# Optimization experiments

Measured on AMD Instinct MI355X. Metric: run time of the kernel, lower is better.

The kernel has to match this reference:

```python
import jax, jax.numpy as jnp
import numpy as np

EPS = 1e-5
QB = 127.0  # int8 activation quantization bound

def rmsnorm(x):
    # SimpleRMSNorm: x / rms(x), no learned scale
    return x * jax.lax.rsqrt(jnp.mean(x * x, axis=-1, keepdims=True) + EPS)

def activation_quant(x):
    # per-token absmax int8 quant-dequant
    scale = QB / jnp.clip(jnp.max(jnp.abs(x), axis=-1, keepdims=True), EPS)
    return jnp.clip(jnp.round(x * scale), -QB - 1, QB) / scale

def weight_quant(w):
    # per-tensor ternary quant-dequant (BitNet b1.58)
    scale = 1.0 / jnp.clip(jnp.mean(jnp.abs(w)), EPS)
    return jnp.clip(jnp.round(w * scale), -1.0, 1.0) / scale

def ste(x, q):
    # straight-through estimator: forward uses q, gradient flows to x
    return x + jax.lax.stop_gradient(q - x)

def bitlinear(x, w, b):
    xn = rmsnorm(x)
    xq = ste(xn, activation_quant(xn))
    wq = ste(w, weight_quant(w))
    # x: [b, s, d_in], w: [d_out, d_in] -> [b, s, d_out]
    return jnp.einsum('bsd,od->bso', xq, wq) + b

def setup_inputs() -> dict:
    key = jax.random.key(0)
    k1, k2, k3, k4, k5 = jax.random.split(key, 5)
    dim, inner = 1024, 4096
    x = jax.random.normal(k1, (4, 4096, dim), dtype=jnp.float32)
    w1 = jax.random.normal(k2, (inner, dim), dtype=jnp.float32) * (dim ** -0.5)
    b1 = jax.random.normal(k3, (inner,), dtype=jnp.float32) * 0.02
    w2 = jax.random.normal(k4, (dim, inner), dtype=jnp.float32) * (inner ** -0.5)
    b2 = jax.random.normal(k5, (dim,), dtype=jnp.float32) * 0.02
    return {"x": x, "w1": w1, "b1": b1, "w2": w2, "b2": b2}

def reference(x, w1, b1, w2, b2):
    h = jax.nn.gelu(bitlinear(x, w1, b1), approximate=False)  # torch nn.GELU default = exact erf
    # dropout p=0.0 is identity; post_act_ln disabled
    return bitlinear(h, w2, b2)
```

## Files before the change

### kernel.cpp

```cpp
#include <hip/hip_runtime.h>
#include <hip/hip_bf16.h>

#define TOK   16384
#define DIM   1024
#define INNER 4096
#define EPSF  1e-5f

typedef int v4i __attribute__((ext_vector_type(4)));

static __device__ __forceinline__ void async_copy16(const char* g, char* l) {
    __builtin_amdgcn_global_load_lds(
        (const __attribute__((address_space(1))) unsigned int*)g,
        (__attribute__((address_space(3))) unsigned int*)l, 16, 0, 0);
}

static __device__ __forceinline__ float bf2f(unsigned short u) {
    return __uint_as_float(((unsigned)u) << 16);
}
static __device__ __forceinline__ unsigned short f2bf(float f) {
    unsigned u = __float_as_uint(f);
    return (unsigned short)((u + 0x7fffu + ((u >> 16) & 1u)) >> 16);
}

static __device__ __forceinline__ float fast_erf(float z) {
    float az = fabsf(z);
    float tt = __builtin_amdgcn_rcpf(1.f + 0.3275911f * az);
    float poly = ((((1.061405429f * tt - 1.453152027f) * tt + 1.421413741f) * tt
                   - 0.284496736f) * tt + 0.254829592f) * tt;
    float er = 1.f - poly * __expf(-az * az);
    return copysignf(er, z);
}

static __device__ __forceinline__ float waveSum(float v) {
#pragma unroll
    for (int o = 32; o > 0; o >>= 1) v += __shfl_down(v, o, 64);
    return v;
}
static __device__ __forceinline__ float waveMax(float v) {
#pragma unroll
    for (int o = 32; o > 0; o >>= 1) v = fmaxf(v, __shfl_down(v, o, 64));
    return v;
}

__global__ void absmean_k(const float* __restrict__ w, int n4, float* __restrict__ acc) {
    int idx = blockIdx.x * blockDim.x + threadIdx.x;
    int stride = gridDim.x * blockDim.x;
    const float4* w4 = (const float4*)w;
    float s = 0.f;
    for (int i = idx; i < n4; i += stride) {
        float4 v = w4[i];
        s += fabsf(v.x) + fabsf(v.y) + fabsf(v.z) + fabsf(v.w);
    }
    __shared__ float sp[4];
    int wv = threadIdx.x >> 6, lane = threadIdx.x & 63;
    s = waveSum(s);
    if (lane == 0) sp[wv] = s;
    __syncthreads();
    if (threadIdx.x == 0) atomicAdd(acc, sp[0] + sp[1] + sp[2] + sp[3]);
}

__global__ void wquant_k(const float* __restrict__ w, int n,
                         const float* __restrict__ acc, float* __restrict__ wscale,
                         char* __restrict__ wq) {
    float mean = *acc / (float)n;
    float cl = fmaxf(mean, EPSF);
    float s = 1.f / cl;
    if (blockIdx.x == 0 && threadIdx.x == 0) *wscale = cl;
    int idx = blockIdx.x * blockDim.x + threadIdx.x;
    int stride = gridDim.x * blockDim.x;
    int n4 = n >> 2;
    const float4* w4 = (const float4*)w;
    unsigned* q4 = (unsigned*)wq;
    for (int i = idx; i < n4; i += stride) {
        float4 v = w4[i];
        float e[4] = {v.x, v.y, v.z, v.w};
        unsigned packed = 0;
#pragma unroll
        for (int j = 0; j < 4; j++) {
            float r = rintf(e[j] * s);
            r = fminf(fmaxf(r, -1.f), 1.f);
            packed |= ((unsigned)((int)r & 0xff)) << (8 * j);
        }
        q4[i] = packed;
    }
}

template <int D, int VPT>
__global__ void actquant_f32_k(const float* __restrict__ X, char* __restrict__ Q,
                               float* __restrict__ rs_out) {
    int token = blockIdx.x;
    int t = threadIdx.x;
    const float4* xp = (const float4*)(X + (long)token * D);
    float vals[VPT];
    float ss = 0.f, am = 0.f;
#pragma unroll
    for (int j = 0; j < VPT / 4; j++) {
        float4 v = xp[t * (VPT / 4) + j];
        vals[4 * j] = v.x; vals[4 * j + 1] = v.y; vals[4 * j + 2] = v.z; vals[4 * j + 3] = v.w;
        ss += v.x * v.x + v.y * v.y + v.z * v.z + v.w * v.w;
        am = fmaxf(am, fmaxf(fmaxf(fabsf(v.x), fabsf(v.y)), fmaxf(fabsf(v.z), fabsf(v.w))));
    }
    __shared__ float sp[8];
    __shared__ float bc[2];
    int wv = t >> 6, lane = t & 63;
    float S = waveSum(ss);
    float M = waveMax(am);
    if (lane == 0) { sp[wv] = S; sp[4 + wv] = M; }
    __syncthreads();
    if (t == 0) {
        float Sa = sp[0] + sp[1] + sp[2] + sp[3];
        float Ma = fmaxf(fmaxf(sp[4], sp[5]), fmaxf(sp[6], sp[7]));
        float rinv = rsqrtf(Sa * (1.f / (float)D) + EPSF);
        float amn = Ma * rinv;
        float scale = 127.f / fmaxf(amn, EPSF);
        rs_out[token] = 1.f / scale;
        bc[0] = rinv; bc[1] = scale;
    }
    __syncthreads();
    float rinv = bc[0], scale = bc[1];
    unsigned outw[VPT / 4];
#pragma unroll
    for (int j = 0; j < VPT; j++) {
        float r = rintf((vals[j] * rinv) * scale);
        r = fminf(fmaxf(r, -128.f), 127.f);
        unsigned qi = (unsigned)((int)r & 0xff) << (8 * (j & 3));
        if ((j & 3) == 0) outw[j / 4] = qi; else outw[j / 4] |= qi;
    }
    unsigned* qp = (unsigned*)(Q + (long)token * D);
#pragma unroll
    for (int j = 0; j < VPT / 4; j++) qp[t * (VPT / 4) + j] = outw[j];
}

template <int D, int VPT>
__global__ void actquant_bf16_k(const unsigned short* __restrict__ X, char* __restrict__ Q,
                                float* __restrict__ rs_out) {
    int token = blockIdx.x;
    int t = threadIdx.x;
    const unsigned* x2 = (const unsigned*)(X + (long)token * D);
    float vals[VPT];
    float ss = 0.f, am = 0.f;
#pragma unroll
    for (int j = 0; j < VPT / 2; j++) {
        unsigned v = x2[t * (VPT / 2) + j];
        float f0 = bf2f((unsigned short)(v & 0xffff));
        float f1 = bf2f((unsigned short)(v >> 16));
        vals[2 * j] = f0; vals[2 * j + 1] = f1;
        ss += f0 * f0 + f1 * f1;
        am = fmaxf(am, fmaxf(fabsf(f0), fabsf(f1)));
    }
    __shared__ float sp[8];
    __shared__ float bc[2];
    int wv = t >> 6, lane = t & 63;
    float S = waveSum(ss);
    float M = waveMax(am);
    if (lane == 0) { sp[wv] = S; sp[4 + wv] = M; }
    __syncthreads();
    if (t == 0) {
        float Sa = sp[0] + sp[1] + sp[2] + sp[3];
        float Ma = fmaxf(fmaxf(sp[4], sp[5]), fmaxf(sp[6], sp[7]));
        float rinv = rsqrtf(Sa * (1.f / (float)D) + EPSF);
        float amn = Ma * rinv;
        float scale = 127.f / fmaxf(amn, EPSF);
        rs_out[token] = 1.f / scale;
        bc[0] = rinv; bc[1] = scale;
    }
    __syncthreads();
    float rinv = bc[0], scale = bc[1];
    unsigned outw[VPT / 4];
#pragma unroll
    for (int j = 0; j < VPT; j++) {
        float r = rintf((vals[j] * rinv) * scale);
        r = fminf(fmaxf(r, -128.f), 127.f);
        unsigned qi = (unsigned)((int)r & 0xff) << (8 * (j & 3));
        if ((j & 3) == 0) outw[j / 4] = qi; else outw[j / 4] |= qi;
    }
    unsigned* qp = (unsigned*)(Q + (long)token * D);
#pragma unroll
    for (int j = 0; j < VPT / 4; j++) qp[t * (VPT / 4) + j] = outw[j];
}

template <int DO_GELU, int OUT_F32>
__global__ __launch_bounds__(256) void gemm_i8_k(
    const char* __restrict__ A, const char* __restrict__ Bw,
    const float* __restrict__ rs, const float* __restrict__ wscale_p,
    const float* __restrict__ bias, void* __restrict__ outp,
    int M, int N, int K) {
    __shared__ char As[2][8192];
    __shared__ char Bs[2][8192];
    int t = threadIdx.x;
    int n0 = blockIdx.x * 128, m0 = blockIdx.y * 128;
    int wv = t >> 6, lane = t & 63, lm = lane & 15, q = lane >> 4;
    int wrow = (wv >> 1) * 64, wcol = (wv & 1) * 64;

    int r = t >> 2;
    int csrc = (t & 3) ^ (r & 3);
    const char* Ap = A + (long)(m0 + r) * K + csrc * 16;
    const char* Bp = Bw + (long)(n0 + r) * K + csrc * 16;
    long rowoff = (long)64 * K;

    v4i acc[4][4] = {};
    int aidx[4], bidx[4];
#pragma unroll
    for (int i = 0; i < 4; i++) {
        int ml = wrow + i * 16 + lm;
        aidx[i] = ml * 4 + (q ^ (ml & 3));
        int nl = wcol + i * 16 + lm;
        bidx[i] = nl * 4 + (q ^ (nl & 3));
    }

    auto issue = [&](int it, int buf) {
        long k0 = (long)it << 6;
        async_copy16(Ap + k0,          As[buf] + t * 16);
        async_copy16(Ap + rowoff + k0, As[buf] + 4096 + t * 16);
        async_copy16(Bp + k0,          Bs[buf] + t * 16);
        async_copy16(Bp + rowoff + k0, Bs[buf] + 4096 + t * 16);
    };

    int nIt = K >> 6;
    issue(0, 0);
    for (int it = 0; it < nIt; ++it) {
        int cur = it & 1;
        if (it + 1 < nIt) {
            issue(it + 1, cur ^ 1);
            asm volatile("s_waitcnt vmcnt(4)" ::: "memory");
        } else {
            asm volatile("s_waitcnt vmcnt(0)" ::: "memory");
        }
        asm volatile("s_barrier" ::: "memory");
        const v4i* As4 = (const v4i*)As[cur];
        const v4i* Bs4 = (const v4i*)Bs[cur];
        v4i a[4], b[4];
#pragma unroll
        for (int i = 0; i < 4; i++) { a[i] = As4[aidx[i]]; b[i] = Bs4[bidx[i]]; }
#pragma unroll
        for (int i = 0; i < 4; i++)
#pragma unroll
            for (int j = 0; j < 4; j++)
                acc[i][j] = __builtin_amdgcn_mfma_i32_16x16x64_i8(a[i], b[j], acc[i][j], 0, 0, 0);
        asm volatile("s_barrier" ::: "memory");
    }

    float wsc = *wscale_p;
#pragma unroll
    for (int i = 0; i < 4; i++) {
        int mg = m0 + wrow + i * 16 + q * 4;
        float fs[4];
#pragma unroll
        for (int rr = 0; rr < 4; rr++) fs[rr] = rs[mg + rr] * wsc;
#pragma unroll
        for (int j = 0; j < 4; j++) {
            int ng = n0 + wcol + j * 16 + lm;
            float bv = bias[ng];
#pragma unroll
            for (int rr = 0; rr < 4; rr++) {
                float v = (float)acc[i][j][rr] * fs[rr] + bv;
                if (DO_GELU) v = 0.5f * v * (1.f + fast_erf(v * 0.70710678118654752f));
                long idx = (long)(mg + rr) * N + ng;
                if (OUT_F32) ((float*)outp)[idx] = v;
                else ((unsigned short*)outp)[idx] = f2bf(v);
            }
        }
    }
}

extern "C" void kernel_launch(void* const* d_in, const int* in_sizes, int n_in,
                              void* d_out, int out_size, void* d_ws, size_t ws_size,
                              hipStream_t stream) {
    const float* x  = (const float*)d_in[0];
    const float* w1 = (const float*)d_in[1];
    const float* b1 = (const float*)d_in[2];
    const float* w2 = (const float*)d_in[3];
    const float* b2 = (const float*)d_in[4];
    float* out = (float*)d_out;

    char* ws = (char*)d_ws;
    float* acc1 = (float*)(ws + 0);
    float* acc2 = (float*)(ws + 4);
    float* wsc1 = (float*)(ws + 8);
    float* wsc2 = (float*)(ws + 12);
    size_t off = 256;
    char* w1q = ws + off; off += (size_t)INNER * DIM;
    char* w2q = ws + off; off += (size_t)INNER * DIM;
    char* xq1 = ws + off; off += (size_t)TOK * DIM;
    float* rs1 = (float*)(ws + off); off += (size_t)TOK * 4;
    char* xq2 = ws + off; off += (size_t)TOK * INNER;
    float* rs2 = (float*)(ws + off); off += (size_t)TOK * 4;
    unsigned short* h = (unsigned short*)(ws + off);

    hipMemsetAsync(d_ws, 0, 16, stream);

    int nw = INNER * DIM;
    absmean_k<<<1024, 256, 0, stream>>>(w1, nw / 4, acc1);
    absmean_k<<<1024, 256, 0, stream>>>(w2, nw / 4, acc2);
    wquant_k<<<2048, 256, 0, stream>>>(w1, nw, acc1, wsc1, w1q);
    wquant_k<<<2048, 256, 0, stream>>>(w2, nw, acc2, wsc2, w2q);

    actquant_f32_k<DIM, 4><<<TOK, 256, 0, stream>>>(x, xq1, rs1);
    gemm_i8_k<1, 0><<<dim3(INNER / 128, TOK / 128), 256, 0, stream>>>(
        xq1, w1q, rs1, wsc1, b1, (void*)h, TOK, INNER, DIM);
    actquant_bf16_k<INNER, 16><<<TOK, 256, 0, stream>>>(h, xq2, rs2);
    gemm_i8_k<0, 1><<<dim3(DIM / 128, TOK / 128), 256, 0, stream>>>(
        xq2, w2q, rs2, wsc2, b2, (void*)out, TOK, DIM, INNER);
}
```

Measured before the change: 440.0 us.

## Enlarge int8 GEMM tile to 256x128 using 32x32x32 MFMA and vectorize actquant IO

The int8 GEMM tile grows from 128x128 to 256x128, and each wave now computes a 128x64 subtile with 32x32x32 i8 MFMAs instead of 16x16x64. The LDS swizzle and the async copy pattern change to match the larger A tile. This raises arithmetic intensity and reuse of the B tile, at the cost of more accumulator registers and more LDS, and it halves the number of blocks. The bf16 activation-quant kernel also switches to 16-byte vector loads and stores.

```diff
diff --git a/kernel.cpp b/kernel.cpp
--- a/kernel.cpp
+++ b/kernel.cpp
@@ -6,7 +6,8 @@
 #define INNER 4096
 #define EPSF  1e-5f
 
-typedef int v4i __attribute__((ext_vector_type(4)));
+typedef int v4i  __attribute__((ext_vector_type(4)));
+typedef int v16i __attribute__((ext_vector_type(16)));
 
 static __device__ __forceinline__ void async_copy16(const char* g, char* l) {
     __builtin_amdgcn_global_load_lds(
@@ -136,17 +137,21 @@
                                 float* __restrict__ rs_out) {
     int token = blockIdx.x;
     int t = threadIdx.x;
-    const unsigned* x2 = (const unsigned*)(X + (long)token * D);
+    const uint4* xp = (const uint4*)(X + (long)token * D);
     float vals[VPT];
     float ss = 0.f, am = 0.f;
 #pragma unroll
-    for (int j = 0; j < VPT / 2; j++) {
-        unsigned v = x2[t * (VPT / 2) + j];
-        float f0 = bf2f((unsigned short)(v & 0xffff));
-        float f1 = bf2f((unsigned short)(v >> 16));
-        vals[2 * j] = f0; vals[2 * j + 1] = f1;
-        ss += f0 * f0 + f1 * f1;
-        am = fmaxf(am, fmaxf(fabsf(f0), fabsf(f1)));
+    for (int j = 0; j < VPT / 8; j++) {
+        uint4 v = xp[t * (VPT / 8) + j];
+        unsigned ws[4] = {v.x, v.y, v.z, v.w};
+#pragma unroll
+        for (int p = 0; p < 4; p++) {
+            float f0 = bf2f((unsigned short)(ws[p] & 0xffff));
+            float f1 = bf2f((unsigned short)(ws[p] >> 16));
+            vals[8 * j + 2 * p] = f0; vals[8 * j + 2 * p + 1] = f1;
+            ss += f0 * f0 + f1 * f1;
+            am = fmaxf(am, fmaxf(fabsf(f0), fabsf(f1)));
+        }
     }
     __shared__ float sp[8];
     __shared__ float bc[2];
@@ -166,7 +171,7 @@
     }
     __syncthreads();
     float rinv = bc[0], scale = bc[1];
-    unsigned outw[VPT / 4];
+    unsigned outw[4];
 #pragma unroll
     for (int j = 0; j < VPT; j++) {
         float r = rintf((vals[j] * rinv) * scale);
@@ -174,46 +179,63 @@
         unsigned qi = (unsigned)((int)r & 0xff) << (8 * (j & 3));
         if ((j & 3) == 0) outw[j / 4] = qi; else outw[j / 4] |= qi;
     }
-    unsigned* qp = (unsigned*)(Q + (long)token * D);
-#pragma unroll
-    for (int j = 0; j < VPT / 4; j++) qp[t * (VPT / 4) + j] = outw[j];
+    uint4* qp = (uint4*)(Q + (long)token * D);
+    qp[t] = make_uint4(outw[0], outw[1], outw[2], outw[3]);
 }
 
 template <int DO_GELU, int OUT_F32>
-__global__ __launch_bounds__(256) void gemm_i8_k(
+__global__ __launch_bounds__(256, 2) void gemm_i8_k(
     const char* __restrict__ A, const char* __restrict__ Bw,
     const float* __restrict__ rs, const float* __restrict__ wscale_p,
     const float* __restrict__ bias, void* __restrict__ outp,
     int M, int N, int K) {
-    __shared__ char As[2][8192];
+    __shared__ char As[2][16384];
     __shared__ char Bs[2][8192];
     int t = threadIdx.x;
-    int n0 = blockIdx.x * 128, m0 = blockIdx.y * 128;
-    int wv = t >> 6, lane = t & 63, lm = lane & 15, q = lane >> 4;
-    int wrow = (wv >> 1) * 64, wcol = (wv & 1) * 64;
+    int n0 = blockIdx.x * 128, m0 = blockIdx.y * 256;
+    int wv = t >> 6, lane = t & 63;
+    int l31 = lane & 31, kh = lane >> 5;
+    int wm = (wv & 1) * 128, wn = (wv >> 1) * 64;
 
     int r = t >> 2;
-    int csrc = (t & 3) ^ (r & 3);
-    const char* Ap = A + (long)(m0 + r) * K + csrc * 16;
-    const char* Bp = Bw + (long)(n0 + r) * K + csrc * 16;
-    long rowoff = (long)64 * K;
-
-    v4i acc[4][4] = {};
-    int aidx[4], bidx[4];
+    const char* aps[4];
+    const char* bps[2];
+#pragma unroll
+    for (int c = 0; c < 4; c++) {
+        int row = c * 64 + r;
+        int src = (t & 3) ^ ((row >> 1) & 3);
+        aps[c] = A + (long)(m0 + row) * K + src * 16;
+    }
+#pragma unroll
+    for (int c = 0; c < 2; c++) {
+        int row = c * 64 + r;
+        int src = (t & 3) ^ ((row >> 1) & 3);
+        bps[c] = Bw + (long)(n0 + row) * K + src * 16;
+    }
+
+    v16i acc[4][2] = {};
+    int aidx[4][2], bidx[2][2];
 #pragma unroll
     for (int i = 0; i < 4; i++) {
-        int ml = wrow + i * 16 + lm;
-        aidx[i] = ml * 4 + (q ^ (ml & 3));
-        int nl = wcol + i * 16 + lm;
-        bidx[i] = nl * 4 + (q ^ (nl & 3));
+        int row = wm + i * 32 + l31;
+        int sw = (row >> 1) & 3;
+#pragma unroll
+        for (int ks = 0; ks < 2; ks++) aidx[i][ks] = row * 4 + ((ks * 2 + kh) ^ sw);
+    }
+#pragma unroll
+    for (int j = 0; j < 2; j++) {
+        int row = wn + j * 32 + l31;
+        int sw = (row >> 1) & 3;
+#pragma unroll
+        for (int ks = 0; ks < 2; ks++) bidx[j][ks] = row * 4 + ((ks * 2 + kh) ^ sw);
     }
 
     auto issue = [&](int it, int buf) {
         long k0 = (long)it << 6;
-        async_copy16(Ap + k0,          As[buf] + t * 16);
-        async_copy16(Ap + rowoff + k0, As[buf] + 4096 + t * 16);
-        async_copy16(Bp + k0,          Bs[buf] + t * 16);
-        async_copy16(Bp + rowoff + k0, Bs[buf] + 4096 + t * 16);
+#pragma unroll
+        for (int c = 0; c < 4; c++) async_copy16(aps[c] + k0, As[buf] + c * 4096 + t * 16);
+#pragma unroll
+        for (int c = 0; c < 2; c++) async_copy16(bps[c] + k0, Bs[buf] + c * 4096 + t * 16);
     };
 
     int nIt = K >> 6;
@@ -222,40 +244,49 @@
         int cur = it & 1;
         if (it + 1 < nIt) {
             issue(it + 1, cur ^ 1);
-            asm volatile("s_waitcnt vmcnt(4)" ::: "memory");
+            asm volatile("s_waitcnt vmcnt(6)" ::: "memory");
         } else {
             asm volatile("s_waitcnt vmcnt(0)" ::: "memory");
         }
         asm volatile("s_barrier" ::: "memory");
         const v4i* As4 = (const v4i*)As[cur];
         const v4i* Bs4 = (const v4i*)Bs[cur];
-        v4i a[4], b[4];
-#pragma unroll
-        for (int i = 0; i < 4; i++) { a[i] = As4[aidx[i]]; b[i] = Bs4[bidx[i]]; }
-#pragma unroll
-        for (int i = 0; i < 4; i++)
-#pragma unroll
-            for (int j = 0; j < 4; j++)
-                acc[i][j] = __builtin_amdgcn_mfma_i32_16x16x64_i8(a[i], b[j], acc[i][j], 0, 0, 0);
+#pragma unroll
+        for (int ks = 0; ks < 2; ks++) {
+            v4i a[4], b[2];
+#pragma unroll
+            for (int i = 0; i < 4; i++) a[i] = As4[aidx[i][ks]];
+#pragma unroll
+            for (int j = 0; j < 2; j++) b[j] = Bs4[bidx[j][ks]];
+#pragma unroll
+            for (int i = 0; i < 4; i++)
+#pragma unroll
+                for (int j = 0; j < 2; j++)
+                    acc[i][j] = __builtin_amdgcn_mfma_i32_32x32x32_i8(a[i], b[j], acc[i][j], 0, 0, 0);
+        }
         asm volatile("s_barrier" ::: "memory");
     }
 
     float wsc = *wscale_p;
+    float bv[2];
+#pragma unroll
+    for (int j = 0; j < 2; j++) bv[j] = bias[n0 + wn + j * 32 + l31];
 #pragma unroll
     for (int i = 0; i < 4; i++) {
-        int mg = m0 + wrow + i * 16 + q * 4;
-        float fs[4];
-#pragma unroll
-        for (int rr = 0; rr < 4; rr++) fs[rr] = rs[mg + rr] * wsc;
-#pragma unroll
-        for (int j = 0; j < 4; j++) {
-            int ng = n0 + wcol + j * 16 + lm;
-            float bv = bias[ng];
-#pragma unroll
-            for (int rr = 0; rr < 4; rr++) {
-                float v = (float)acc[i][j][rr] * fs[rr] + bv;
+        int mbase = m0 + wm + i * 32 + 4 * kh;
+        float fsv[16];
+#pragma unroll
+        for (int rg = 0; rg < 16; rg++)
+            fsv[rg] = rs[mbase + (rg & 3) + 8 * (rg >> 2)] * wsc;
+#pragma unroll
+        for (int j = 0; j < 2; j++) {
+            int ng = n0 + wn + j * 32 + l31;
+#pragma unroll
+            for (int rg = 0; rg < 16; rg++) {
+                int mg = mbase + (rg & 3) + 8 * (rg >> 2);
+                float v = (float)acc[i][j][rg] * fsv[rg] + bv[j];
                 if (DO_GELU) v = 0.5f * v * (1.f + fast_erf(v * 0.70710678118654752f));
-                long idx = (long)(mg + rr) * N + ng;
+                long idx = (long)mg * N + ng;
                 if (OUT_F32) ((float*)outp)[idx] = v;
                 else ((unsigned short*)outp)[idx] = f2bf(v);
             }
@@ -296,9 +327,9 @@
     wquant_k<<<2048, 256, 0, stream>>>(w2, nw, acc2, wsc2, w2q);
 
     actquant_f32_k<DIM, 4><<<TOK, 256, 0, stream>>>(x, xq1, rs1);
-    gemm_i8_k<1, 0><<<dim3(INNER / 128, TOK / 128), 256, 0, stream>>>(
+    gemm_i8_k<1, 0><<<dim3(INNER / 128, TOK / 256), 256, 0, stream>>>(
         xq1, w1q, rs1, wsc1, b1, (void*)h, TOK, INNER, DIM);
     actquant_bf16_k<INNER, 16><<<TOK, 256, 0, stream>>>(h, xq2, rs2);
-    gemm_i8_k<0, 1><<<dim3(DIM / 128, TOK / 128), 256, 0, stream>>>(
+    gemm_i8_k<0, 1><<<dim3(DIM / 128, TOK / 256), 256, 0, stream>>>(
         xq2, w2q, rs2, wsc2, b2, (void*)out, TOK, DIM, INNER);
 }
```

Result: faster. 419.5 us (-4.7%).
